# Kernel tuning notes

Measured on AMD Instinct MI355X. Metric: run time of the kernel, lower is better.

The kernel has to match this reference:

```python
import jax, jax.numpy as jnp
import numpy as np

H = 128   # hidden_size
DYN = 2   # dynamic_features


def setup_inputs() -> dict:
    B, S, STAT = 256, 64, 2
    key = jax.random.key(0)
    ks = jax.random.split(key, 9)
    sc = 0.05
    return {
        "static": jax.random.normal(ks[0], (B, STAT, S), jnp.float32),
        "static_embeddings": jax.random.normal(ks[1], (B, H, S), jnp.float32),
        "dynamic": jax.random.uniform(ks[2], (B, DYN, S), jnp.float32),
        # dynamic_embedding: Conv1d(2 -> 128, k=1)
        "dyn_w": jax.random.normal(ks[3], (H, DYN), jnp.float32) * sc,
        "dyn_b": jnp.zeros((H,), jnp.float32),
        # decoder_input_dynamic_embedding: Conv1d(128 -> 128, k=1)
        "in_w": jax.random.normal(ks[4], (H, H), jnp.float32) * sc,
        "in_b": jnp.zeros((H,), jnp.float32),
        # GRU (single layer, batch_first), torch gate order r,z,n
        "w_ih": jax.random.normal(ks[5], (3 * H, H), jnp.float32) * sc,
        "w_hh": jax.random.normal(ks[6], (3 * H, H), jnp.float32) * sc,
        "b_ih": jnp.zeros((3 * H,), jnp.float32),
        "b_hh": jnp.zeros((3 * H,), jnp.float32),
        # DoubleAttention: scores = v . tanh(W [static; dynamic; hidden])
        "W_att": jax.random.normal(ks[7], (H, 3 * H), jnp.float32) * sc,
        "v_att": jax.random.normal(ks[8], (H,), jnp.float32) * sc,
    }


def _pointer_forward(static_embeddings, dynamic, dyn_w, dyn_b, in_w, in_b,
                     w_ih, w_hh, b_ih, b_hh, W_att, v_att):
    B, Hd, S = static_embeddings.shape
    NEG = jnp.asarray(-1e9, static_embeddings.dtype)
    base = jax.random.key(42)

    def gru_cell(x, h):  # torch nn.GRU single step
        gi = x @ w_ih.T + b_ih
        gh = h @ w_hh.T + b_hh
        ir, iz, i_n = jnp.split(gi, 3, axis=-1)
        hr, hz, h_n = jnp.split(gh, 3, axis=-1)
        r = jax.nn.sigmoid(ir + hr)
        z = jax.nn.sigmoid(iz + hz)
        n = jnp.tanh(i_n + r * h_n)
        return (1.0 - z) * n + z * h

    first_mask = jnp.zeros((B, S), static_embeddings.dtype).at[:, 0].set(1.0)

    def step(carry, i):
        dec_in, h, visited, dyn = carry
        # decoder_input_dynamic_embedding: 1x1 conv == per-token linear
        x = dec_in @ in_w.T + in_b                      # [B,H]
        h = gru_cell(x, h)                              # decoder_output == new hidden
        # i==0: only depot (index 0) is selectable; afterwards: unvisited nodes
        mask = jnp.where(i == 0, first_mask, 1.0 - visited)
        dyn_emb = jnp.einsum('bds,hd->bhs', dyn, dyn_w) + dyn_b[None, :, None]
        ctx = jnp.concatenate(
            [static_embeddings, dyn_emb,
             jnp.broadcast_to(h[:, :, None], (B, Hd, S))], axis=1)  # [B,3H,S]
        scores = jnp.einsum('h,bhs->bs', v_att,
                            jnp.tanh(jnp.einsum('hk,bks->bhs', W_att, ctx)))
        logits = jnp.where(mask > 0, scores, NEG)       # -inf on masked positions
        ptr = jax.random.categorical(jax.random.fold_in(base, i), logits)  # sample
        logp = jnp.take_along_axis(jax.nn.log_softmax(logits, -1),
                                   ptr[:, None], axis=1)[:, 0]
        sel = (jnp.arange(S)[None, :] == ptr[:, None]).astype(dyn.dtype)  # [B,S]
        visited = jnp.maximum(visited, sel)
        dyn = dyn * (1.0 - sel)[:, None, :]             # update_dynamic_state
        # original feeds the (conv-transformed) decoder input back to itself
        return (x, h, visited, dyn), (ptr, logp)

    init = (static_embeddings[:, :, 0],                  # decoder_input = emb of node 0
            jnp.zeros((B, Hd), static_embeddings.dtype),  # GRU hidden
            jnp.zeros((B, S), static_embeddings.dtype),   # visited
            dynamic)
    _, (tours, logps) = jax.lax.scan(step, init, jnp.arange(S))
    return tours.T, logps.T  # [B,S], [B,S]


def reference(static, static_embeddings, dynamic, dyn_w, dyn_b, in_w, in_b,
              w_ih, w_hh, b_ih, b_hh, W_att, v_att):
    # dropout layers are identity in eval mode; `static` is only used for logging
    return _pointer_forward(static_embeddings, dynamic, dyn_w, dyn_b, in_w, in_b,
                            w_ih, w_hh, b_ih, b_hh, W_att, v_att)
```

## Files before the change

### kernel.cpp

```cpp
#include <hip/hip_runtime.h>
#include <stdint.h>


#define BN 256
#define SN 64
#define HN 128
#define NEGV (-1.0e9f)
#define TINYF 1.17549435e-38f

#define PIN(x) asm volatile("" : "+v"(x))
#define PIN4(v) asm volatile("" : "+v"(v.x), "+v"(v.y), "+v"(v.z), "+v"(v.w))

#define OFF_A   0
#define OFF_GI  8192
#define OFF_WHC 8192
#define OFF_SET 16384
#define OFF_UT  24832
#define OFF_HC  33280
#define OFF_KK  33536
#define OFF_SV  33664
#define OFF_DY  33792
#define OFF_WD  33920
#define OFF_CV  34176
#define SMEM_FLOATS 34304

__device__ __forceinline__ uint32_t rotl32(uint32_t v, int d) {
  return (v << d) | (v >> (32 - d));
}

__device__ __forceinline__ void threefry2x32(uint32_t k0, uint32_t k1,
                                             uint32_t x0, uint32_t x1,
                                             uint32_t& o0, uint32_t& o1) {
  uint32_t ks2 = k0 ^ k1 ^ 0x1BD11BDAu;
  x0 += k0; x1 += k1;
  x0 += x1; x1 = rotl32(x1, 13); x1 ^= x0;
  x0 += x1; x1 = rotl32(x1, 15); x1 ^= x0;
  x0 += x1; x1 = rotl32(x1, 26); x1 ^= x0;
  x0 += x1; x1 = rotl32(x1, 6);  x1 ^= x0;
  x0 += k1; x1 += ks2 + 1u;
  x0 += x1; x1 = rotl32(x1, 17); x1 ^= x0;
  x0 += x1; x1 = rotl32(x1, 29); x1 ^= x0;
  x0 += x1; x1 = rotl32(x1, 16); x1 ^= x0;
  x0 += x1; x1 = rotl32(x1, 24); x1 ^= x0;
  x0 += ks2; x1 += k0 + 2u;
  x0 += x1; x1 = rotl32(x1, 13); x1 ^= x0;
  x0 += x1; x1 = rotl32(x1, 15); x1 ^= x0;
  x0 += x1; x1 = rotl32(x1, 26); x1 ^= x0;
  x0 += x1; x1 = rotl32(x1, 6);  x1 ^= x0;
  x0 += k0; x1 += k1 + 3u;
  x0 += x1; x1 = rotl32(x1, 17); x1 ^= x0;
  x0 += x1; x1 = rotl32(x1, 29); x1 ^= x0;
  x0 += x1; x1 = rotl32(x1, 16); x1 ^= x0;
  x0 += x1; x1 = rotl32(x1, 24); x1 ^= x0;
  x0 += k1; x1 += ks2 + 4u;
  x0 += x1; x1 = rotl32(x1, 13); x1 ^= x0;
  x0 += x1; x1 = rotl32(x1, 15); x1 ^= x0;
  x0 += x1; x1 = rotl32(x1, 26); x1 ^= x0;
  x0 += x1; x1 = rotl32(x1, 6);  x1 ^= x0;
  x0 += ks2; x1 += k0 + 5u;
  o0 = x0; o1 = x1;
}

__device__ __forceinline__ float jax_gumbel(uint32_t k0, uint32_t k1, int j) {
  uint32_t o0, o1;
  threefry2x32(k0, k1, 0u, (uint32_t)j, o0, o1);
  uint32_t bits = o0 ^ o1;
  uint32_t ub = (bits >> 9) | 0x3F800000u;
  float u = __uint_as_float(ub) - 1.0f;
  u = fmaxf(u + TINYF, TINYF);
  return -logf(-logf(u));
}

__device__ __forceinline__ float ftanh(float x) {
  float ax = fabsf(x);
  float e = __expf(-2.0f * ax);
  float r = (1.0f - e) * __builtin_amdgcn_rcpf(1.0f + e);
  return copysignf(r, x);
}

__device__ __forceinline__ float fsig(float x) {
  return __builtin_amdgcn_rcpf(1.0f + __expf(-x));
}

__global__ void k0_dyn(const float* __restrict__ W_att, const float* __restrict__ dyn_w,
                       const float* __restrict__ dyn_b, float* __restrict__ Wd,
                       float* __restrict__ cv) {
  int h = threadIdx.x;
  float w0 = 0.f, w1 = 0.f, cc = 0.f;
  for (int k = 0; k < HN; ++k) {
    float w = W_att[h * 384 + 128 + k];
    w0 = fmaf(w, dyn_w[2 * k + 0], w0);
    w1 = fmaf(w, dyn_w[2 * k + 1], w1);
    cc = fmaf(w, dyn_b[k], cc);
  }
  Wd[2 * h] = w0; Wd[2 * h + 1] = w1; cv[h] = cc;
}

__global__ __launch_bounds__(512)
__attribute__((amdgpu_waves_per_eu(2, 2)))
void mega(
    const float* __restrict__ SE, const float* __restrict__ dynamic,
    const float* __restrict__ in_w, const float* __restrict__ in_b,
    const float* __restrict__ w_ih, const float* __restrict__ b_ih,
    const float* __restrict__ w_hh, const float* __restrict__ b_hh,
    const float* __restrict__ W_att, const float* __restrict__ v_att,
    const float* __restrict__ Wd, const float* __restrict__ cv,
    float* __restrict__ out) {
  extern __shared__ float sm[];
  int b = blockIdx.x, t = threadIdx.x;
  float* A   = sm + OFF_A;
  float* GIl = sm + OFF_GI;
  float* WHC = sm + OFF_WHC;
  float* SET = sm + OFF_SET;
  float* UT  = sm + OFF_UT;
  float* HC  = sm + OFF_HC;
  uint32_t* KK = (uint32_t*)(sm + OFF_KK);
  float* SV  = sm + OFF_SV;
  float* DY  = sm + OFF_DY;
  float* WDs = sm + OFF_WD;
  float* CVs = sm + OFF_CV;

  if (t < 64) {
    uint32_t o0, o1;
    threefry2x32(0u, 42u, 0u, (uint32_t)t, o0, o1);
    KK[2 * t] = o0; KK[2 * t + 1] = o1;
  }
  if (t < 128) {
    SV[t]  = v_att[t];
    DY[t]  = dynamic[b * 128 + t];
    CVs[t] = cv[t];
    HC[t]  = SE[b * 8192 + t * 64];
  }
  if (t < 256) WDs[t] = Wd[t];
  __syncthreads();

  {
    int ml = t >> 2, ks = t & 3;
    float4 wv[8];
#pragma unroll
    for (int q = 0; q < 8; ++q) {
      wv[q] = *(const float4*)(in_w + ml * HN + q * 16 + ks * 4);
      PIN4(wv[q]);
    }
    float bib = in_b[ml];
    for (int ii = 0; ii < SN; ++ii) {
      const float* xc = HC + (ii & 1) * 128;
      float* xn = HC + ((ii + 1) & 1) * 128;
      float a0 = 0.f, a1 = 0.f, a2 = 0.f, a3 = 0.f;
#pragma unroll
      for (int q = 0; q < 8; ++q) {
        float4 x4 = *(const float4*)(xc + q * 16 + ks * 4);
        a0 = fmaf(wv[q].x, x4.x, a0);
        a1 = fmaf(wv[q].y, x4.y, a1);
        a2 = fmaf(wv[q].z, x4.z, a2);
        a3 = fmaf(wv[q].w, x4.w, a3);
      }
      float s = (a0 + a1) + (a2 + a3);
      s += __shfl_xor(s, 1); s += __shfl_xor(s, 2);
      if (ks == 0) {
        float xv = s + bib;
        A[ii * 128 + ml] = xv;
        xn[ml] = xv;
      }
      __syncthreads();
    }
  }

  {
    int ml = t >> 2, ks = t & 3;
    float4 wv[3][8]; float bi[3];
#pragma unroll
    for (int j = 0; j < 3; ++j) {
#pragma unroll
      for (int q = 0; q < 8; ++q) {
        wv[j][q] = *(const float4*)(w_ih + (ml + 128 * j) * HN + q * 16 + ks * 4);
        PIN4(wv[j][q]);
      }
      bi[j] = b_ih[ml + 128 * j];
    }
    for (int n = 0; n < SN; ++n) {
      float4 x4[8];
#pragma unroll
      for (int q = 0; q < 8; ++q)
        x4[q] = *(const float4*)(A + n * 128 + q * 16 + ks * 4);
      float sum[3];
#pragma unroll
      for (int j = 0; j < 3; ++j) {
        float a0 = 0.f, a1 = 0.f, a2 = 0.f, a3 = 0.f;
#pragma unroll
        for (int q = 0; q < 8; ++q) {
          a0 = fmaf(wv[j][q].x, x4[q].x, a0);
          a1 = fmaf(wv[j][q].y, x4[q].y, a1);
          a2 = fmaf(wv[j][q].z, x4[q].z, a2);
          a3 = fmaf(wv[j][q].w, x4[q].w, a3);
        }
        float s = (a0 + a1) + (a2 + a3);
        s += __shfl_xor(s, 1); s += __shfl_xor(s, 2);
        sum[j] = s + bi[j];
      }
      if (ks == 0) {
#pragma unroll
        for (int j = 0; j < 3; ++j) GIl[n * 384 + ml + 128 * j] = sum[j];
      }
    }
    __syncthreads();
  }

  if (t < 256) HC[t] = 0.f;
  __syncthreads();
  {
    int ml = t >> 2, ks = t & 3;
    float4 wv[3][8]; float bh[3];
#pragma unroll
    for (int j = 0; j < 3; ++j) {
#pragma unroll
      for (int q = 0; q < 8; ++q) {
        wv[j][q] = *(const float4*)(w_hh + (ml + 128 * j) * HN + q * 16 + ks * 4);
        PIN4(wv[j][q]);
      }
      bh[j] = b_hh[ml + 128 * j];
    }
    float hp = 0.f;
    for (int ii = 0; ii < SN; ++ii) {
      const float* hcr = HC + (ii & 1) * 128;
      float* hcw = HC + ((ii + 1) & 1) * 128;
      float4 x4[8];
#pragma unroll
      for (int q = 0; q < 8; ++q)
        x4[q] = *(const float4*)(hcr + q * 16 + ks * 4);
      float sum[3];
#pragma unroll
      for (int j = 0; j < 3; ++j) {
        float a0 = 0.f, a1 = 0.f, a2 = 0.f, a3 = 0.f;
#pragma unroll
        for (int q = 0; q < 8; ++q) {
          a0 = fmaf(wv[j][q].x, x4[q].x, a0);
          a1 = fmaf(wv[j][q].y, x4[q].y, a1);
          a2 = fmaf(wv[j][q].z, x4[q].z, a2);
          a3 = fmaf(wv[j][q].w, x4[q].w, a3);
        }
        float s = (a0 + a1) + (a2 + a3);
        s += __shfl_xor(s, 1); s += __shfl_xor(s, 2);
        sum[j] = s + bh[j];
      }
      if (ks == 0) {
        const float* gr = GIl + ii * 384;
        float r = fsig(gr[ml] + sum[0]);
        float z = fsig(gr[128 + ml] + sum[1]);
        float nn = ftanh(gr[256 + ml] + r * sum[2]);
        float hn = (1.0f - z) * nn + z * hp;
        hcw[ml] = hn;
        A[ii * 128 + ml] = hn;
        hp = hn;
      }
      __syncthreads();
    }
  }

  {
    int ml = t >> 3, ks = t & 7;
    float4 w0[4], w1[4];
#pragma unroll
    for (int q = 0; q < 4; ++q) {
      w0[q] = *(const float4*)(W_att + (ml)      * 384 + 256 + q * 32 + ks * 4);
      w1[q] = *(const float4*)(W_att + (ml + 64) * 384 + 256 + q * 32 + ks * 4);
      PIN4(w0[q]); PIN4(w1[q]);
    }
    for (int n = 0; n < SN; ++n) {
      float4 x4[4];
#pragma unroll
      for (int q = 0; q < 4; ++q)
        x4[q] = *(const float4*)(A + n * 128 + q * 32 + ks * 4);
      float a00 = 0.f, a01 = 0.f, a10 = 0.f, a11 = 0.f;
#pragma unroll
      for (int q = 0; q < 4; ++q) {
        a00 = fmaf(w0[q].x, x4[q].x, a00);
        a01 = fmaf(w0[q].y, x4[q].y, a01);
        a00 = fmaf(w0[q].z, x4[q].z, a00);
        a01 = fmaf(w0[q].w, x4[q].w, a01);
        a10 = fmaf(w1[q].x, x4[q].x, a10);
        a11 = fmaf(w1[q].y, x4[q].y, a11);
        a10 = fmaf(w1[q].z, x4[q].z, a10);
        a11 = fmaf(w1[q].w, x4[q].w, a11);
      }
      float s0 = a00 + a01, s1 = a10 + a11;
      s0 += __shfl_xor(s0, 1); s0 += __shfl_xor(s0, 2); s0 += __shfl_xor(s0, 4);
      s1 += __shfl_xor(s1, 1); s1 += __shfl_xor(s1, 2); s1 += __shfl_xor(s1, 4);
      if (ks == 0) { WHC[n * 128 + ml] = s0; WHC[n * 128 + ml + 64] = s1; }
    }
    __syncthreads();
  }

  for (int p = 0; p < 16; ++p) {
    int idx = p * 512 + t;
    int h = idx >> 6, s = idx & 63;
    SET[s * 132 + h] = SE[b * 8192 + idx];
  }
  __syncthreads();

  {
    int ml = t >> 3, ks = t & 7;
    float4 w0[4], w1[4];
#pragma unroll
    for (int q = 0; q < 4; ++q) {
      w0[q] = *(const float4*)(W_att + (ml)      * 384 + q * 32 + ks * 4);
      w1[q] = *(const float4*)(W_att + (ml + 64) * 384 + q * 32 + ks * 4);
      PIN4(w0[q]); PIN4(w1[q]);
    }
    for (int n = 0; n < SN; ++n) {
      float4 x4[4];
#pragma unroll
      for (int q = 0; q < 4; ++q)
        x4[q] = *(const float4*)(SET + n * 132 + q * 32 + ks * 4);
      float a00 = 0.f, a01 = 0.f, a10 = 0.f, a11 = 0.f;
#pragma unroll
      for (int q = 0; q < 4; ++q) {
        a00 = fmaf(w0[q].x, x4[q].x, a00);
        a01 = fmaf(w0[q].y, x4[q].y, a01);
        a00 = fmaf(w0[q].z, x4[q].z, a00);
        a01 = fmaf(w0[q].w, x4[q].w, a01);
        a10 = fmaf(w1[q].x, x4[q].x, a10);
        a11 = fmaf(w1[q].y, x4[q].y, a11);
        a10 = fmaf(w1[q].z, x4[q].z, a10);
        a11 = fmaf(w1[q].w, x4[q].w, a11);
      }
      float s0 = a00 + a01, s1 = a10 + a11;
      s0 += __shfl_xor(s0, 1); s0 += __shfl_xor(s0, 2); s0 += __shfl_xor(s0, 4);
      s1 += __shfl_xor(s1, 1); s1 += __shfl_xor(s1, 2); s1 += __shfl_xor(s1, 4);
      if (ks == 0) {
        float d0 = DY[n], d1 = DY[64 + n];
        UT[(ml)      * 66 + n] = s0 + WDs[2 * ml] * d0 + WDs[2 * ml + 1] * d1 + CVs[ml];
        UT[(ml + 64) * 66 + n] = s1 + WDs[2 * (ml + 64)] * d0 + WDs[2 * (ml + 64) + 1] * d1 + CVs[ml + 64];
      }
    }
    __syncthreads();
  }

  {
    int s = t & 63, w = t >> 6;
    float acc[8];
#pragma unroll
    for (int j = 0; j < 8; ++j) acc[j] = 0.f;
    for (int h = 0; h < HN; h += 4) {
      float u0 = UT[(h + 0) * 66 + s];
      float u1 = UT[(h + 1) * 66 + s];
      float u2 = UT[(h + 2) * 66 + s];
      float u3 = UT[(h + 3) * 66 + s];
      float4 v4 = *(const float4*)(SV + h);
#pragma unroll
      for (int j = 0; j < 8; ++j) {
        float4 wh = *(const float4*)(WHC + (w * 8 + j) * 128 + h);
        float a = acc[j];
        a = fmaf(v4.x, ftanh(u0 + wh.x), a);
        a = fmaf(v4.y, ftanh(u1 + wh.y), a);
        a = fmaf(v4.z, ftanh(u2 + wh.z), a);
        a = fmaf(v4.w, ftanh(u3 + wh.w), a);
        acc[j] = a;
      }
    }
    __syncthreads();
#pragma unroll
    for (int j = 0; j < 8; ++j) A[(w * 8 + j) * 64 + s] = acc[j];
    __syncthreads();
  }

  {
    float* G = A + 4096;
    for (int p = 0; p < 8; ++p) {
      int idx = p * 512 + t;
      int i = idx >> 6;
      G[idx] = jax_gumbel(KK[2 * i], KK[2 * i + 1], b * 64 + (idx & 63));
    }
    __syncthreads();
  }

  if (t < 64) {
    const float* Pl = A;
    const float* Gl = A + 4096;
    int s = t;
    bool visited = false;
    for (int i = 0; i < SN; ++i) {
      float score = Pl[i * 64 + s];
      bool allowed = (i == 0) ? (s == 0) : (!visited);
      float logit = allowed ? score : NEGV;
      float z = logit + Gl[i * 64 + s];
      float bz = z; int bi = s;
#pragma unroll
      for (int off = 32; off > 0; off >>= 1) {
        float oz = __shfl_xor(bz, off);
        int oi = __shfl_xor(bi, off);
        if (oz > bz || (oz == bz && oi < bi)) { bz = oz; bi = oi; }
      }
      int ptr = bi;
      float m = logit;
#pragma unroll
      for (int off = 32; off > 0; off >>= 1) m = fmaxf(m, __shfl_xor(m, off));
      float e = expf(logit - m);
      float sum = e;
#pragma unroll
      for (int off = 32; off > 0; off >>= 1) sum += __shfl_xor(sum, off);
      float chosen = __shfl(logit, ptr);
      float logp = (chosen - m) - logf(sum);
      if (s == ptr) visited = true;
      if (s == 0) {
        out[b * SN + i] = (float)ptr;
        out[BN * SN + b * SN + i] = logp;
      }
    }
  }
}

extern "C" void kernel_launch(void* const* d_in, const int* in_sizes, int n_in,
                              void* d_out, int out_size, void* d_ws, size_t ws_size,
                              hipStream_t stream) {
  const float* SE    = (const float*)d_in[1];
  const float* dynam = (const float*)d_in[2];
  const float* dyn_w = (const float*)d_in[3];
  const float* dyn_b = (const float*)d_in[4];
  const float* in_w  = (const float*)d_in[5];
  const float* in_b  = (const float*)d_in[6];
  const float* w_ih  = (const float*)d_in[7];
  const float* w_hh  = (const float*)d_in[8];
  const float* b_ih  = (const float*)d_in[9];
  const float* b_hh  = (const float*)d_in[10];
  const float* W_att = (const float*)d_in[11];
  const float* v_att = (const float*)d_in[12];
  float* out = (float*)d_out;
  float* ws = (float*)d_ws;

  float* Wd = ws;
  float* cv = ws + 256;

  (void)hipFuncSetAttribute((const void*)mega,
                            hipFuncAttributeMaxDynamicSharedMemorySize,
                            SMEM_FLOATS * 4);

  hipLaunchKernelGGL(k0_dyn, dim3(1), dim3(128), 0, stream,
                     W_att, dyn_w, dyn_b, Wd, cv);
  hipLaunchKernelGGL(mega, dim3(BN), dim3(512), SMEM_FLOATS * 4, stream,
                     SE, dynam, in_w, in_b, w_ih, b_ih, w_hh, b_hh,
                     W_att, v_att, Wd, cv, out);
}
```

Baseline: 325.6 us.

## Cut register pressure in GRU phases by splitting weight tiles and reloading half

Removes the inline-asm register pins and the fixed waves-per-EU attribute, using launch_bounds(512,1) instead. The input-gate projection is split into two passes over halves of the K dimension, accumulating through shared memory. The recurrent GRU loop keeps only half of w_hh in registers and reloads the other half from global memory (L1/L2) every timestep. The aim is to lower VGPR use and avoid spills, at the cost of extra memory traffic inside the serial recurrence.

```diff
diff --git a/kernel.cpp b/kernel.cpp
--- a/kernel.cpp
+++ b/kernel.cpp
@@ -7,9 +7,6 @@
 #define HN 128
 #define NEGV (-1.0e9f)
 #define TINYF 1.17549435e-38f
-
-#define PIN(x) asm volatile("" : "+v"(x))
-#define PIN4(v) asm volatile("" : "+v"(v.x), "+v"(v.y), "+v"(v.z), "+v"(v.w))
 
 #define OFF_A   0
 #define OFF_GI  8192
@@ -96,9 +93,7 @@
   Wd[2 * h] = w0; Wd[2 * h + 1] = w1; cv[h] = cc;
 }
 
-__global__ __launch_bounds__(512)
-__attribute__((amdgpu_waves_per_eu(2, 2)))
-void mega(
+__global__ __launch_bounds__(512, 1) void mega(
     const float* __restrict__ SE, const float* __restrict__ dynamic,
     const float* __restrict__ in_w, const float* __restrict__ in_b,
     const float* __restrict__ w_ih, const float* __restrict__ b_ih,
@@ -138,10 +133,8 @@
     int ml = t >> 2, ks = t & 3;
     float4 wv[8];
 #pragma unroll
-    for (int q = 0; q < 8; ++q) {
+    for (int q = 0; q < 8; ++q)
       wv[q] = *(const float4*)(in_w + ml * HN + q * 16 + ks * 4);
-      PIN4(wv[q]);
-    }
     float bib = in_b[ml];
     for (int ii = 0; ii < SN; ++ii) {
       const float* xc = HC + (ii & 1) * 128;
@@ -168,39 +161,43 @@
 
   {
     int ml = t >> 2, ks = t & 3;
-    float4 wv[3][8]; float bi[3];
-#pragma unroll
-    for (int j = 0; j < 3; ++j) {
-#pragma unroll
-      for (int q = 0; q < 8; ++q) {
-        wv[j][q] = *(const float4*)(w_ih + (ml + 128 * j) * HN + q * 16 + ks * 4);
-        PIN4(wv[j][q]);
-      }
-      bi[j] = b_ih[ml + 128 * j];
-    }
-    for (int n = 0; n < SN; ++n) {
-      float4 x4[8];
-#pragma unroll
-      for (int q = 0; q < 8; ++q)
-        x4[q] = *(const float4*)(A + n * 128 + q * 16 + ks * 4);
-      float sum[3];
+#pragma unroll
+    for (int p = 0; p < 2; ++p) {
+      float4 wv[3][4]; float bi[3];
 #pragma unroll
       for (int j = 0; j < 3; ++j) {
-        float a0 = 0.f, a1 = 0.f, a2 = 0.f, a3 = 0.f;
-#pragma unroll
-        for (int q = 0; q < 8; ++q) {
-          a0 = fmaf(wv[j][q].x, x4[q].x, a0);
-          a1 = fmaf(wv[j][q].y, x4[q].y, a1);
-          a2 = fmaf(wv[j][q].z, x4[q].z, a2);
-          a3 = fmaf(wv[j][q].w, x4[q].w, a3);
+#pragma unroll
+        for (int q = 0; q < 4; ++q)
+          wv[j][q] = *(const float4*)(w_ih + (ml + 128 * j) * HN + p * 64 + q * 16 + ks * 4);
+        bi[j] = b_ih[ml + 128 * j];
+      }
+      for (int n = 0; n < SN; ++n) {
+        float4 x4[4];
+#pragma unroll
+        for (int q = 0; q < 4; ++q)
+          x4[q] = *(const float4*)(A + n * 128 + p * 64 + q * 16 + ks * 4);
+        float sum[3];
+#pragma unroll
+        for (int j = 0; j < 3; ++j) {
+          float a0 = 0.f, a1 = 0.f, a2 = 0.f, a3 = 0.f;
+#pragma unroll
+          for (int q = 0; q < 4; ++q) {
+            a0 = fmaf(wv[j][q].x, x4[q].x, a0);
+            a1 = fmaf(wv[j][q].y, x4[q].y, a1);
+            a2 = fmaf(wv[j][q].z, x4[q].z, a2);
+            a3 = fmaf(wv[j][q].w, x4[q].w, a3);
+          }
+          float s = (a0 + a1) + (a2 + a3);
+          s += __shfl_xor(s, 1); s += __shfl_xor(s, 2);
+          sum[j] = s;
         }
-        float s = (a0 + a1) + (a2 + a3);
-        s += __shfl_xor(s, 1); s += __shfl_xor(s, 2);
-        sum[j] = s + bi[j];
-      }
-      if (ks == 0) {
-#pragma unroll
-        for (int j = 0; j < 3; ++j) GIl[n * 384 + ml + 128 * j] = sum[j];
+        if (ks == 0) {
+#pragma unroll
+          for (int j = 0; j < 3; ++j) {
+            int idx = n * 384 + ml + 128 * j;
+            GIl[idx] = (p == 0) ? sum[j] : (GIl[idx] + sum[j] + bi[j]);
+          }
+        }
       }
     }
     __syncthreads();
@@ -210,20 +207,24 @@
   __syncthreads();
   {
     int ml = t >> 2, ks = t & 3;
-    float4 wv[3][8]; float bh[3];
+    float4 wvA[3][4]; float bh[3];
 #pragma unroll
     for (int j = 0; j < 3; ++j) {
 #pragma unroll
-      for (int q = 0; q < 8; ++q) {
-        wv[j][q] = *(const float4*)(w_hh + (ml + 128 * j) * HN + q * 16 + ks * 4);
-        PIN4(wv[j][q]);
-      }
+      for (int q = 0; q < 4; ++q)
+        wvA[j][q] = *(const float4*)(w_hh + (ml + 128 * j) * HN + q * 16 + ks * 4);
       bh[j] = b_hh[ml + 128 * j];
     }
     float hp = 0.f;
     for (int ii = 0; ii < SN; ++ii) {
       const float* hcr = HC + (ii & 1) * 128;
       float* hcw = HC + ((ii + 1) & 1) * 128;
+      float4 wvB[3][4];
+#pragma unroll
+      for (int j = 0; j < 3; ++j)
+#pragma unroll
+        for (int q = 0; q < 4; ++q)
+          wvB[j][q] = *(const float4*)(w_hh + (ml + 128 * j) * HN + 64 + q * 16 + ks * 4);
       float4 x4[8];
 #pragma unroll
       for (int q = 0; q < 8; ++q)
@@ -233,11 +234,18 @@
       for (int j = 0; j < 3; ++j) {
         float a0 = 0.f, a1 = 0.f, a2 = 0.f, a3 = 0.f;
 #pragma unroll
-        for (int q = 0; q < 8; ++q) {
-          a0 = fmaf(wv[j][q].x, x4[q].x, a0);
-          a1 = fmaf(wv[j][q].y, x4[q].y, a1);
-          a2 = fmaf(wv[j][q].z, x4[q].z, a2);
-          a3 = fmaf(wv[j][q].w, x4[q].w, a3);
+        for (int q = 0; q < 4; ++q) {
+          a0 = fmaf(wvA[j][q].x, x4[q].x, a0);
+          a1 = fmaf(wvA[j][q].y, x4[q].y, a1);
+          a2 = fmaf(wvA[j][q].z, x4[q].z, a2);
+          a3 = fmaf(wvA[j][q].w, x4[q].w, a3);
+        }
+#pragma unroll
+        for (int q = 0; q < 4; ++q) {
+          a0 = fmaf(wvB[j][q].x, x4[q + 4].x, a0);
+          a1 = fmaf(wvB[j][q].y, x4[q + 4].y, a1);
+          a2 = fmaf(wvB[j][q].z, x4[q + 4].z, a2);
+          a3 = fmaf(wvB[j][q].w, x4[q + 4].w, a3);
         }
         float s = (a0 + a1) + (a2 + a3);
         s += __shfl_xor(s, 1); s += __shfl_xor(s, 2);
@@ -264,7 +272,6 @@
     for (int q = 0; q < 4; ++q) {
       w0[q] = *(const float4*)(W_att + (ml)      * 384 + 256 + q * 32 + ks * 4);
       w1[q] = *(const float4*)(W_att + (ml + 64) * 384 + 256 + q * 32 + ks * 4);
-      PIN4(w0[q]); PIN4(w1[q]);
     }
     for (int n = 0; n < SN; ++n) {
       float4 x4[4];
@@ -305,7 +312,6 @@
     for (int q = 0; q < 4; ++q) {
       w0[q] = *(const float4*)(W_att + (ml)      * 384 + q * 32 + ks * 4);
       w1[q] = *(const float4*)(W_att + (ml + 64) * 384 + q * 32 + ks * 4);
-      PIN4(w0[q]); PIN4(w1[q]);
     }
     for (int n = 0; n < SN; ++n) {
       float4 x4[4];
```

After: 334.3 us. 1.03x slower.
